# Kernel optimization log

Hardware: AMD Instinct MI355X
Metric: run time of the kernel (lower is better)

The kernel has to match this reference:

```python
import jax, jax.numpy as jnp
import numpy as np

B, C, H, W = 16, 512, 64, 64
K = 5  # k_size for channel=512: int(abs((log2(512)+1)/2)) = 5, already odd


def setup_inputs() -> dict:
    key = jax.random.key(0)
    k1, k2, k3, k4 = jax.random.split(key, 4)
    x = jax.random.normal(k1, (B, C, H, W), dtype=jnp.float32)
    w1x1 = jax.random.normal(k2, (C, C), dtype=jnp.float32) * (1.0 / np.sqrt(C))
    b1x1 = jax.random.normal(k3, (C,), dtype=jnp.float32) * 0.01
    w1d = jax.random.normal(k4, (C, K), dtype=jnp.float32) * (1.0 / np.sqrt(K))
    return {"x": x, "w1x1": w1x1, "b1x1": b1x1, "w1d": w1d}


def reference(x, w1x1, b1x1, w1d):
    b, c, h, w = x.shape
    # conv1x1 (pointwise) + softmax over all c*h*w elements per batch.
    # NOTE: y is computed but unused in the original module's return; kept for fidelity.
    y = jnp.einsum('bchw,oc->bohw', x, w1x1) + b1x1[None, :, None, None]
    y = jax.nn.softmax(y.reshape(b, -1), axis=1).reshape(b, c, h, w)
    del y
    # channel attention: global average pool -> per-channel conv1d on a length-1 slice.
    z = x.mean(axis=(2, 3))  # (b, c)
    k = w1d.shape[1]
    center = (k - 1) // 2
    # Each Conv1d sees a zero-padded length-k window with z_i at the center tap,
    # so out_i = sum_j W_i[j] * pad(z_i)[j] = W_i[center] * z_i. Implement the
    # full dot against the padded window (identical math, vectorized over channels).
    zpad = jnp.zeros((b, c, k), dtype=x.dtype).at[:, :, center].set(z)
    zc = jnp.einsum('bck,ck->bc', zpad, w1d)
    gate = jax.nn.sigmoid(zc)[:, :, None, None]  # (b, c, 1, 1)
    return x * gate
```

## Files before the change

kernel.cpp:

```cpp
#include <hip/hip_runtime.h>


#define NC 512
#define HW 4096
#define PER_LANE 16

typedef float vf4 __attribute__((ext_vector_type(4)));

__global__ __launch_bounds__(256) void mcanet_gate_kernel(
    const float* __restrict__ x,
    const float* __restrict__ w1d,
    float* __restrict__ out)
{
    const int wave  = threadIdx.x >> 6;
    const int lane  = threadIdx.x & 63;
    const int plane = (blockIdx.x << 2) + wave;
    const int c = plane & (NC - 1);

    const float wc = w1d[c * 5 + 2];

    const long long base = (long long)plane * HW;
    const vf4* __restrict__ xin = (const vf4*)(x + base);
    vf4* __restrict__ o = (vf4*)(out + base);

    vf4 v[PER_LANE];
    #pragma unroll
    for (int i = 0; i < PER_LANE; ++i)
        v[i] = __builtin_nontemporal_load(xin + lane + (i << 6));

    vf4 acc = v[0];
    #pragma unroll
    for (int i = 1; i < PER_LANE; ++i)
        acc += v[i];
    float s = (acc.x + acc.y) + (acc.z + acc.w);

    #pragma unroll
    for (int off = 32; off > 0; off >>= 1)
        s += __shfl_xor(s, off, 64);

    const float zc = wc * (s * (1.0f / (float)HW));
    const float g  = 1.0f / (1.0f + __expf(-zc));

    #pragma unroll
    for (int i = 0; i < PER_LANE; ++i) {
        vf4 r = v[i] * g;
        __builtin_nontemporal_store(r, o + lane + (i << 6));
    }
}

extern "C" void kernel_launch(void* const* d_in, const int* in_sizes, int n_in,
                              void* d_out, int out_size, void* d_ws, size_t ws_size,
                              hipStream_t stream) {
    const float* x   = (const float*)d_in[0];
    const float* w1d = (const float*)d_in[3];
    float* out = (float*)d_out;

    const int planes = 16 * NC;
    mcanet_gate_kernel<<<planes / 4, 256, 0, stream>>>(x, w1d, out);
}
```

Baseline: 225.3 us.

## Split gate computation into separate mean and scale kernels

Replaces the single fused kernel, which read each plane once and held it in registers, with two kernels. The first computes per-plane means and sigmoid gates into workspace. The second rereads x and scales it with finer-grained waves. This cuts register pressure and raises parallelism in the scale pass, but reads x twice (128 MB becomes 256 MB) and adds a launch boundary. The second read may hit in the large last-level cache.

Result: slower. 251.2 us (+11.5%).

```diff
diff --git a/kernel.cpp b/kernel.cpp
--- a/kernel.cpp
+++ b/kernel.cpp
@@ -7,43 +7,50 @@
 
 typedef float vf4 __attribute__((ext_vector_type(4)));
 
-__global__ __launch_bounds__(256) void mcanet_gate_kernel(
+__global__ __launch_bounds__(256) void mcanet_mean_kernel(
     const float* __restrict__ x,
     const float* __restrict__ w1d,
-    float* __restrict__ out)
+    float* __restrict__ gates)
 {
-    const int wave  = threadIdx.x >> 6;
     const int lane  = threadIdx.x & 63;
-    const int plane = (blockIdx.x << 2) + wave;
-    const int c = plane & (NC - 1);
+    const int plane = (blockIdx.x << 2) + (threadIdx.x >> 6);
 
-    const float wc = w1d[c * 5 + 2];
+    const vf4* __restrict__ xin = (const vf4*)(x + (long long)plane * HW);
 
-    const long long base = (long long)plane * HW;
-    const vf4* __restrict__ xin = (const vf4*)(x + base);
-    vf4* __restrict__ o = (vf4*)(out + base);
-
-    vf4 v[PER_LANE];
-    #pragma unroll
-    for (int i = 0; i < PER_LANE; ++i)
-        v[i] = __builtin_nontemporal_load(xin + lane + (i << 6));
-
-    vf4 acc = v[0];
+    vf4 acc = xin[lane];
     #pragma unroll
     for (int i = 1; i < PER_LANE; ++i)
-        acc += v[i];
+        acc += xin[lane + (i << 6)];
     float s = (acc.x + acc.y) + (acc.z + acc.w);
 
     #pragma unroll
     for (int off = 32; off > 0; off >>= 1)
         s += __shfl_xor(s, off, 64);
 
-    const float zc = wc * (s * (1.0f / (float)HW));
-    const float g  = 1.0f / (1.0f + __expf(-zc));
+    if (lane == 0) {
+        const float wc = w1d[(plane & (NC - 1)) * 5 + 2];
+        const float zc = wc * (s * (1.0f / (float)HW));
+        gates[plane] = 1.0f / (1.0f + __expf(-zc));
+    }
+}
+
+__global__ __launch_bounds__(256) void mcanet_scale_kernel(
+    const float* __restrict__ x,
+    const float* __restrict__ gates,
+    float* __restrict__ out)
+{
+    const int lane = threadIdx.x & 63;
+    const int wave = (blockIdx.x << 2) + (threadIdx.x >> 6);
+
+    const float g = gates[wave >> 1];
+
+    const long long base = (long long)wave * (HW / 2);
+    const vf4* __restrict__ xin = (const vf4*)(x + base);
+    vf4* __restrict__ o = (vf4*)(out + base);
 
     #pragma unroll
-    for (int i = 0; i < PER_LANE; ++i) {
-        vf4 r = v[i] * g;
+    for (int i = 0; i < 8; ++i) {
+        vf4 r = xin[lane + (i << 6)] * g;
         __builtin_nontemporal_store(r, o + lane + (i << 6));
     }
 }
@@ -53,8 +60,10 @@
                               hipStream_t stream) {
     const float* x   = (const float*)d_in[0];
     const float* w1d = (const float*)d_in[3];
-    float* out = (float*)d_out;
+    float* out   = (float*)d_out;
+    float* gates = (float*)d_ws;
 
     const int planes = 16 * NC;
-    mcanet_gate_kernel<<<planes / 4, 256, 0, stream>>>(x, w1d, out);
+    mcanet_mean_kernel<<<planes / 4, 256, 0, stream>>>(x, w1d, gates);
+    mcanet_scale_kernel<<<planes / 2, 256, 0, stream>>>(x, gates, out);
 }
```
